# Kernel optimization log

Measured on AMD Instinct MI355X. Metric: run time of the kernel, lower is better.

The kernel has to match this reference:

```python
import jax, jax.numpy as jnp
import numpy as np

KH, KW = 7, 7      # t2t kernel_size
ST = 3             # stride
PD = 3             # padding
K = KH * KW        # 49 taps per patch


def _patch_indices(H, W):
    """Linear indices into the padded (Hp,Wp) image for every (patch l, tap k)."""
    Hp, Wp = H + 2 * PD, W + 2 * PD
    oh = (H + 2 * PD - KH) // ST + 1
    ow = (W + 2 * PD - KW) // ST + 1
    ki, kj = np.meshgrid(np.arange(KH), np.arange(KW), indexing='ij')
    rows = (np.arange(oh) * ST)[:, None, None, None] + ki[None, None]   # (oh,1,kh,kw)
    cols = (np.arange(ow) * ST)[None, :, None, None] + kj[None, None]   # (1,ow,kh,kw)
    idx = (rows * Wp + cols).reshape(oh * ow, K)                        # (L, 49)
    return jnp.asarray(idx), Hp, Wp, oh * ow


def setup_inputs() -> dict:
    key = jax.random.key(0)
    k1, k2, k3 = jax.random.split(key, 3)
    b, n, d, hd = 2, 5760, 512, 1960
    return {
        'x': jax.random.normal(k1, (b, n, d), dtype=jnp.float32),
        'W1': jax.random.normal(k2, (d, hd), dtype=jnp.float32) * 0.02,
        'b1': jnp.zeros((hd,), dtype=jnp.float32),
        'W2': jax.random.normal(k3, (hd, d), dtype=jnp.float32) * 0.02,
        'b2': jnp.zeros((d,), dtype=jnp.float32),
        'out_h': 60,
        'out_w': 108,
    }


def reference(x, W1, b1, W2, b2, out_h, out_w):
    H, W = int(out_h), int(out_w)
    idx, Hp, Wp, L = _patch_indices(H, W)          # idx: (L, 49)
    idxf = idx.reshape(-1)                         # (L*49,)

    b, n, _ = x.shape
    h = x @ W1 + b1                                # (b, n, 1960)
    hd = h.shape[-1]
    C = hd // K                                    # 40 fold channels
    Bp = (b * n) // L                              # fold batch (= b * t)

    # fold input layout: (Bp, C, K, L) -> scatter-add into padded image
    patches = h.reshape(Bp, L, C, K)
    vals = jnp.transpose(patches, (0, 2, 1, 3)).reshape(Bp * C, L * K)
    img = jnp.zeros((Bp * C, Hp * Wp), x.dtype).at[:, idxf].add(vals)

    # overlap-count normalizer (fold of ones), same for every batch/channel
    count = jnp.zeros((Hp * Wp,), x.dtype).at[idxf].add(jnp.ones_like(idxf, x.dtype))

    # crop padding (as F.fold does), normalize, re-pad with zeros (as F.unfold does)
    img = img.reshape(Bp, C, Hp, Wp)[:, :, PD:PD + H, PD:PD + W]
    cnt = count.reshape(Hp, Wp)[PD:PD + H, PD:PD + W]
    img = img / cnt
    flat = jnp.pad(img, ((0, 0), (0, 0), (PD, PD), (PD, PD))).reshape(Bp * C, Hp * Wp)

    # unfold: gather the same taps back, restore (b, n, hd) token layout
    g = flat[:, idxf].reshape(Bp, C, L, K)
    g = jnp.transpose(g, (0, 2, 1, 3)).reshape(b, n, hd)

    return jax.nn.gelu(g, approximate=False) @ W2 + b2
```

## Files before the change

### kernel.cpp

```cpp
#include <hip/hip_runtime.h>

typedef _Float16 f16;
typedef __attribute__((ext_vector_type(8))) _Float16 half8;
typedef __attribute__((ext_vector_type(4))) _Float16 half4;
typedef __attribute__((ext_vector_type(4))) float f32x4;

#define LDS_AS __attribute__((address_space(3)))
#define GLB_AS __attribute__((address_space(1)))

__device__ __forceinline__ void load16_lds(const f16* g, f16* l) {
    __builtin_amdgcn_global_load_lds((GLB_AS void*)(g), (LDS_AS void*)(l), 16, 0, 0);
}

#define WAIT4_BARRIER()  asm volatile("s_waitcnt vmcnt(4)\n\ts_barrier" ::: "memory")
#define WAIT0_BARRIER()  asm volatile("s_waitcnt vmcnt(0)\n\ts_barrier" ::: "memory")
#define PLAIN_BARRIER()  asm volatile("s_barrier" ::: "memory")

__global__ __launch_bounds__(256, 2) void gemm1(
    const f16* __restrict__ A, const f16* __restrict__ Bt,
    const float* __restrict__ bias, f16* __restrict__ C)
{
    const int id  = blockIdx.x;
    const int xcd = id & 7;
    const int r   = id >> 3;
    const int mt  = r & 15;
    const int nt  = xcd + 8 * (r >> 4);
    if (nt >= 90) return;
    const int m0 = mt * 128, n0 = nt * 128;
    const int K = 512, ldc = 11520;

    __shared__ f16 As[2][128 * 32];
    __shared__ f16 Bs[2][128 * 32];
    const int tid  = threadIdx.x;
    const int wave = tid >> 6;
    const int lane = tid & 63;

    const int s0 = tid, s1 = tid + 256;
    const f16* gA0 = A  + (m0 + (s0 >> 2)) * K + (s0 & 3) * 8;
    const f16* gA1 = A  + (m0 + (s1 >> 2)) * K + (s1 & 3) * 8;
    const f16* gB0 = Bt + (n0 + (s0 >> 2)) * K + (s0 & 3) * 8;
    const f16* gB1 = Bt + (n0 + (s1 >> 2)) * K + (s1 & 3) * 8;

    const int wm = (wave >> 1) * 64;
    const int wn = (wave & 1) * 64;
    const int lr = lane & 15;
    const int k8 = (lane >> 4) * 8;

    f32x4 acc[4][4];
#pragma unroll
    for (int i = 0; i < 4; ++i)
#pragma unroll
        for (int j = 0; j < 4; ++j) acc[i][j] = f32x4{0.f, 0.f, 0.f, 0.f};

#define G1_ISSUE(st, k0) do { \
    load16_lds(gA0 + (k0), &As[st][wave * 512]); \
    load16_lds(gA1 + (k0), &As[st][2048 + wave * 512]); \
    load16_lds(gB0 + (k0), &Bs[st][wave * 512]); \
    load16_lds(gB1 + (k0), &Bs[st][2048 + wave * 512]); \
} while (0)

    G1_ISSUE(0, 0);
    const int NS = 16;
    for (int s = 0; s < NS; ++s) {
        const int cur = s & 1;
        if (s + 1 < NS) {
            G1_ISSUE(cur ^ 1, (s + 1) * 32);
            WAIT4_BARRIER();
        } else {
            WAIT0_BARRIER();
        }
        half8 af[4], bf[4];
#pragma unroll
        for (int i = 0; i < 4; ++i)
            af[i] = *(const half8*)&As[cur][(wm + i * 16 + lr) * 32 + k8];
#pragma unroll
        for (int j = 0; j < 4; ++j)
            bf[j] = *(const half8*)&Bs[cur][(wn + j * 16 + lr) * 32 + k8];
#pragma unroll
        for (int i = 0; i < 4; ++i)
#pragma unroll
            for (int j = 0; j < 4; ++j)
                acc[i][j] = __builtin_amdgcn_mfma_f32_16x16x32_f16(
                    af[i], bf[j], acc[i][j], 0, 0, 0);
        PLAIN_BARRIER();
    }

#pragma unroll
    for (int i = 0; i < 4; ++i) {
#pragma unroll
        for (int rr = 0; rr < 4; ++rr) {
            const int row = m0 + wm + i * 16 + (lane >> 4) * 4 + rr;
            const float bvr = (row < 1960) ? bias[row] : 0.f;
#pragma unroll
            for (int j = 0; j < 4; ++j) {
                const int col = n0 + wn + j * 16 + lr;
                C[row * ldc + col] = (f16)(acc[i][j][rr] + bvr);
            }
        }
    }
}

__global__ __launch_bounds__(512, 2) void gemm2(
    const f16* __restrict__ A, const f16* __restrict__ Bt,
    const float* __restrict__ bias, float* __restrict__ Cout)
{
    const int id  = blockIdx.x;
    const int xcd = id & 7;
    const int j2  = id >> 3;
    const int nt  = j2 & 3;
    const int mt  = (j2 >> 2) * 8 + xcd;
    if (mt >= 90) return;
    const int m0 = mt * 128, n0 = nt * 128;

    __shared__ f16 smem[32768];
    const int tid  = threadIdx.x;
    const int half = tid >> 8;
    const int t    = tid & 255;
    const int wave = (tid >> 6) & 3;
    const int lane = tid & 63;

    const int kbase = half * 1024;
    const int s1 = t + 256;
    const f16* gA0 = A  + (m0 + (t  >> 2)) * 2048 + kbase + (t  & 3) * 8;
    const f16* gA1 = A  + (m0 + (s1 >> 2)) * 2048 + kbase + (s1 & 3) * 8;
    const f16* gB0 = Bt + (n0 + (t  >> 2)) * 2048 + kbase + (t  & 3) * 8;
    const f16* gB1 = Bt + (n0 + (s1 >> 2)) * 2048 + kbase + (s1 & 3) * 8;
    f16* hb = &smem[half * 16384];

    const int wm = (wave >> 1) * 64;
    const int wn = (wave & 1) * 64;
    const int lr = lane & 15;
    const int k8 = (lane >> 4) * 8;

    f32x4 acc[4][4];
#pragma unroll
    for (int i = 0; i < 4; ++i)
#pragma unroll
        for (int j = 0; j < 4; ++j) acc[i][j] = f32x4{0.f, 0.f, 0.f, 0.f};

#define G2_ISSUE(st, k0) do { \
    f16* sb = hb + (st) * 8192; \
    load16_lds(gA0 + (k0), sb + wave * 512); \
    load16_lds(gA1 + (k0), sb + 2048 + wave * 512); \
    load16_lds(gB0 + (k0), sb + 4096 + wave * 512); \
    load16_lds(gB1 + (k0), sb + 6144 + wave * 512); \
} while (0)

    G2_ISSUE(0, 0);
    const int NS = 32;
    for (int s = 0; s < NS; ++s) {
        const int cur = s & 1;
        if (s + 1 < NS) {
            G2_ISSUE(cur ^ 1, (s + 1) * 32);
            WAIT4_BARRIER();
        } else {
            WAIT0_BARRIER();
        }
        const f16* sa = hb + cur * 8192;
        const f16* sbB = sa + 4096;
        half8 af[4], bf[4];
#pragma unroll
        for (int i = 0; i < 4; ++i)
            af[i] = *(const half8*)&sa[(wm + i * 16 + lr) * 32 + k8];
#pragma unroll
        for (int j = 0; j < 4; ++j)
            bf[j] = *(const half8*)&sbB[(wn + j * 16 + lr) * 32 + k8];
#pragma unroll
        for (int i = 0; i < 4; ++i)
#pragma unroll
            for (int j = 0; j < 4; ++j)
                acc[i][j] = __builtin_amdgcn_mfma_f32_16x16x32_f16(
                    af[i], bf[j], acc[i][j], 0, 0, 0);
        PLAIN_BARRIER();
    }

    float* accl = (float*)smem;
    if (half == 1) {
#pragma unroll
        for (int i = 0; i < 4; ++i)
#pragma unroll
            for (int rr = 0; rr < 4; ++rr) {
                const int row = wm + i * 16 + (lane >> 4) * 4 + rr;
#pragma unroll
                for (int j = 0; j < 4; ++j)
                    accl[row * 128 + wn + j * 16 + lr] = acc[i][j][rr];
            }
    }
    __syncthreads();
    if (half == 0) {
#pragma unroll
        for (int j = 0; j < 4; ++j) {
            const int col = wn + j * 16 + lr;
            const float bv = bias[n0 + col];
#pragma unroll
            for (int i = 0; i < 4; ++i) {
#pragma unroll
                for (int rr = 0; rr < 4; ++rr) {
                    const int row = wm + i * 16 + (lane >> 4) * 4 + rr;
                    Cout[(m0 + row) * 512 + n0 + col] =
                        acc[i][j][rr] + accl[row * 128 + col] + bv;
                }
            }
        }
    }
}

__global__ void fold_gelu(const f16* __restrict__ h_t, f16* __restrict__ imgG)
{
    const int r  = blockIdx.x;
    const int bc = blockIdx.y;
    const int bp  = bc / 40;
    const int cch = bc % 40;
    const int c = threadIdx.x;
    if (c >= 114) return;
    float outv = 0.f;
    if (r >= 3 && r < 63 && c >= 3 && c < 111) {
        const int qr = r / 3, rm = r % 3;
        const int qc = c / 3, cm = c % 3;
        int kis[3], ohs[3], nr = 0;
        int kjs[3], ows[3], nc = 0;
#pragma unroll
        for (int t = 0; t < 3; ++t) {
            const int ki = rm + 3 * t, oh = qr - t;
            if (ki < 7 && oh >= 0 && oh < 20) { kis[nr] = ki; ohs[nr] = oh; ++nr; }
            const int kj = cm + 3 * t, ow = qc - t;
            if (kj < 7 && ow >= 0 && ow < 36) { kjs[nc] = kj; ows[nc] = ow; ++nc; }
        }
        float sum = 0.f;
        for (int a = 0; a < nr; ++a)
            for (int b = 0; b < nc; ++b) {
                const int n = cch * 49 + kis[a] * 7 + kjs[b];
                const int token = bp * 720 + ohs[a] * 36 + ows[b];
                sum += (float)h_t[n * 11520 + token];
            }
        const float xv = sum / (float)(nr * nc);
        outv = 0.5f * xv * (1.f + erff(xv * 0.70710678118654752f));
    }
    imgG[(bc * 66 + r) * 114 + c] = (f16)outv;
}

__global__ __launch_bounds__(256) void unfold_lds(
    const f16* __restrict__ imgG, f16* __restrict__ g16)
{
    __shared__ f16 ch[7524];
    const int bc = blockIdx.x;
    const int bp = bc / 40, cch = bc % 40;
    const float* src = (const float*)(imgG + bc * 7524);
    float* dst = (float*)ch;
    for (int i = threadIdx.x; i < 3762; i += 256) dst[i] = src[i];
    __syncthreads();
    const int tokbase = bp * 720;
    const int colbase = cch * 49;
    for (int flat = threadIdx.x; flat < 35280; flat += 256) {
        const int l = flat / 49, k = flat - l * 49;
        const int oh = l / 36, ow = l - oh * 36;
        const int ki = k / 7,  kj = k - ki * 7;
        g16[(tokbase + l) * 2048 + colbase + k] =
            ch[(oh * 3 + ki) * 114 + ow * 3 + kj];
    }
    if (cch >= 36) {
        const int cb = 1960 + (cch - 36) * 22;
        for (int flat = threadIdx.x; flat < 720 * 22; flat += 256) {
            const int l = flat / 22, k = flat - l * 22;
            g16[(tokbase + l) * 2048 + cb + k] = (f16)0.f;
        }
    }
}

__global__ void cvt_x(const float* __restrict__ x, f16* __restrict__ xh, int n4)
{
    const int i = blockIdx.x * 256 + threadIdx.x;
    if (i < n4) {
        const float4 v = ((const float4*)x)[i];
        half4 o;
        o[0] = (f16)v.x; o[1] = (f16)v.y; o[2] = (f16)v.z; o[3] = (f16)v.w;
        ((half4*)xh)[i] = o;
    }
}

__global__ void transpose_pad(const float* __restrict__ src, f16* __restrict__ dst,
                              int R, int C, int Rp, int Cp)
{
    __shared__ float tile[32][33];
    const int r0 = blockIdx.x * 32, c0 = blockIdx.y * 32;
    const int tx = threadIdx.x, ty = threadIdx.y;
#pragma unroll
    for (int i = 0; i < 32; i += 8) {
        const int r = r0 + ty + i, c = c0 + tx;
        tile[ty + i][tx] = (r < R && c < C) ? src[r * C + c] : 0.f;
    }
    __syncthreads();
#pragma unroll
    for (int i = 0; i < 32; i += 8) {
        const int c = c0 + ty + i, r = r0 + tx;
        if (c < Cp && r < Rp) dst[c * Rp + r] = (f16)tile[tx][ty + i];
    }
}

extern "C" void kernel_launch(void* const* d_in, const int* in_sizes, int n_in,
                              void* d_out, int out_size, void* d_ws, size_t ws_size,
                              hipStream_t stream)
{
    const float* x  = (const float*)d_in[0];
    const float* W1 = (const float*)d_in[1];
    const float* b1 = (const float*)d_in[2];
    const float* W2 = (const float*)d_in[3];
    const float* b2 = (const float*)d_in[4];

    char* ws = (char*)d_ws;
    f16* xh   = (f16*)(ws);
    f16* W1t  = (f16*)(ws + 11796480);
    f16* W2t  = (f16*)(ws + 11796480 + 2097152);
    f16* hbuf = (f16*)(ws + 11796480 + 2 * 2097152);
    f16* imgG = (f16*)(ws + 11796480 + 2 * 2097152 + 47185920);

    cvt_x<<<dim3(5760), dim3(256), 0, stream>>>(x, xh, 1474560);
    transpose_pad<<<dim3(16, 64), dim3(32, 8), 0, stream>>>(W1, W1t, 512, 1960, 512, 2048);
    transpose_pad<<<dim3(64, 16), dim3(32, 8), 0, stream>>>(W2, W2t, 1960, 512, 2048, 512);
    gemm1<<<dim3(1536), dim3(256), 0, stream>>>(W1t, xh, b1, hbuf);
    fold_gelu<<<dim3(66, 640), dim3(128), 0, stream>>>(hbuf, imgG);
    unfold_lds<<<dim3(640), dim3(256), 0, stream>>>(imgG, hbuf);
    gemm2<<<dim3(384), dim3(512), 0, stream>>>(hbuf, W2t, b2, (float*)d_out);
}
```

Before: 234.7 us.

## Halve gemm2 N tile, raise occupancy bounds, merge prep kernels into one launch

gemm2 now uses 128x64 output tiles with 768 blocks instead of 128x128 with 384, cutting LDS and accumulator registers per block and raising the launch-bounds occupancy hint. The goal is to fill more CUs and hide latency on a GEMM that otherwise launches few blocks. gemm1's occupancy hint goes from 2 to 3. The x conversion and two weight transposes are merged into one launch to remove launch overhead. The cost is more redundant A-tile loads in gemm2, a simpler block mapping that drops the XCD-aware swizzle, and possible register spills under the tighter bounds.

```diff
diff --git a/kernel.cpp b/kernel.cpp
--- a/kernel.cpp
+++ b/kernel.cpp
@@ -13,10 +13,11 @@
 }
 
 #define WAIT4_BARRIER()  asm volatile("s_waitcnt vmcnt(4)\n\ts_barrier" ::: "memory")
+#define WAIT3_BARRIER()  asm volatile("s_waitcnt vmcnt(3)\n\ts_barrier" ::: "memory")
 #define WAIT0_BARRIER()  asm volatile("s_waitcnt vmcnt(0)\n\ts_barrier" ::: "memory")
 #define PLAIN_BARRIER()  asm volatile("s_barrier" ::: "memory")
 
-__global__ __launch_bounds__(256, 2) void gemm1(
+__global__ __launch_bounds__(256, 3) void gemm1(
     const f16* __restrict__ A, const f16* __restrict__ Bt,
     const float* __restrict__ bias, f16* __restrict__ C)
 {
@@ -100,19 +101,17 @@
     }
 }
 
-__global__ __launch_bounds__(512, 2) void gemm2(
+__global__ __launch_bounds__(512, 4) void gemm2(
     const f16* __restrict__ A, const f16* __restrict__ Bt,
     const float* __restrict__ bias, float* __restrict__ Cout)
 {
-    const int id  = blockIdx.x;
-    const int xcd = id & 7;
-    const int j2  = id >> 3;
-    const int nt  = j2 & 3;
-    const int mt  = (j2 >> 2) * 8 + xcd;
+    const int id = blockIdx.x;
+    const int nt = id / 96;
+    const int mt = id % 96;
     if (mt >= 90) return;
-    const int m0 = mt * 128, n0 = nt * 128;
-
-    __shared__ f16 smem[32768];
+    const int m0 = mt * 128, n0 = nt * 64;
+
+    __shared__ f16 smem[24576];
     const int tid  = threadIdx.x;
     const int half = tid >> 8;
     const int t    = tid & 255;
@@ -124,26 +123,24 @@
     const f16* gA0 = A  + (m0 + (t  >> 2)) * 2048 + kbase + (t  & 3) * 8;
     const f16* gA1 = A  + (m0 + (s1 >> 2)) * 2048 + kbase + (s1 & 3) * 8;
     const f16* gB0 = Bt + (n0 + (t  >> 2)) * 2048 + kbase + (t  & 3) * 8;
-    const f16* gB1 = Bt + (n0 + (s1 >> 2)) * 2048 + kbase + (s1 & 3) * 8;
-    f16* hb = &smem[half * 16384];
+    f16* hb = &smem[half * 12288];
 
     const int wm = (wave >> 1) * 64;
-    const int wn = (wave & 1) * 64;
+    const int wn = (wave & 1) * 32;
     const int lr = lane & 15;
     const int k8 = (lane >> 4) * 8;
 
-    f32x4 acc[4][4];
+    f32x4 acc[4][2];
 #pragma unroll
     for (int i = 0; i < 4; ++i)
 #pragma unroll
-        for (int j = 0; j < 4; ++j) acc[i][j] = f32x4{0.f, 0.f, 0.f, 0.f};
+        for (int j = 0; j < 2; ++j) acc[i][j] = f32x4{0.f, 0.f, 0.f, 0.f};
 
 #define G2_ISSUE(st, k0) do { \
-    f16* sb = hb + (st) * 8192; \
+    f16* sb = hb + (st) * 6144; \
     load16_lds(gA0 + (k0), sb + wave * 512); \
     load16_lds(gA1 + (k0), sb + 2048 + wave * 512); \
     load16_lds(gB0 + (k0), sb + 4096 + wave * 512); \
-    load16_lds(gB1 + (k0), sb + 6144 + wave * 512); \
 } while (0)
 
     G2_ISSUE(0, 0);
@@ -152,23 +149,22 @@
         const int cur = s & 1;
         if (s + 1 < NS) {
             G2_ISSUE(cur ^ 1, (s + 1) * 32);
-            WAIT4_BARRIER();
+            WAIT3_BARRIER();
         } else {
             WAIT0_BARRIER();
         }
-        const f16* sa = hb + cur * 8192;
-        const f16* sbB = sa + 4096;
-        half8 af[4], bf[4];
+        const f16* sa = hb + cur * 6144;
+        half8 af[4], bf[2];
 #pragma unroll
         for (int i = 0; i < 4; ++i)
             af[i] = *(const half8*)&sa[(wm + i * 16 + lr) * 32 + k8];
 #pragma unroll
-        for (int j = 0; j < 4; ++j)
-            bf[j] = *(const half8*)&sbB[(wn + j * 16 + lr) * 32 + k8];
-#pragma unroll
-        for (int i = 0; i < 4; ++i)
-#pragma unroll
-            for (int j = 0; j < 4; ++j)
+        for (int j = 0; j < 2; ++j)
+            bf[j] = *(const half8*)&sa[4096 + (wn + j * 16 + lr) * 32 + k8];
+#pragma unroll
+        for (int i = 0; i < 4; ++i)
+#pragma unroll
+            for (int j = 0; j < 2; ++j)
                 acc[i][j] = __builtin_amdgcn_mfma_f32_16x16x32_f16(
                     af[i], bf[j], acc[i][j], 0, 0, 0);
         PLAIN_BARRIER();
@@ -182,14 +178,14 @@
             for (int rr = 0; rr < 4; ++rr) {
                 const int row = wm + i * 16 + (lane >> 4) * 4 + rr;
 #pragma unroll
-                for (int j = 0; j < 4; ++j)
-                    accl[row * 128 + wn + j * 16 + lr] = acc[i][j][rr];
+                for (int j = 0; j < 2; ++j)
+                    accl[row * 64 + wn + j * 16 + lr] = acc[i][j][rr];
             }
     }
     __syncthreads();
     if (half == 0) {
 #pragma unroll
-        for (int j = 0; j < 4; ++j) {
+        for (int j = 0; j < 2; ++j) {
             const int col = wn + j * 16 + lr;
             const float bv = bias[n0 + col];
 #pragma unroll
@@ -198,7 +194,7 @@
                 for (int rr = 0; rr < 4; ++rr) {
                     const int row = wm + i * 16 + (lane >> 4) * 4 + rr;
                     Cout[(m0 + row) * 512 + n0 + col] =
-                        acc[i][j][rr] + accl[row * 128 + col] + bv;
+                        acc[i][j][rr] + accl[row * 64 + col] + bv;
                 }
             }
         }
@@ -267,23 +263,33 @@
     }
 }
 
-__global__ void cvt_x(const float* __restrict__ x, f16* __restrict__ xh, int n4)
-{
-    const int i = blockIdx.x * 256 + threadIdx.x;
-    if (i < n4) {
+__global__ __launch_bounds__(256) void prep(
+    const float* __restrict__ x, f16* __restrict__ xh,
+    const float* __restrict__ W1, f16* __restrict__ W1t,
+    const float* __restrict__ W2, f16* __restrict__ W2t)
+{
+    __shared__ float tile[32][33];
+    const int b = blockIdx.x, t = threadIdx.x;
+    if (b < 5760) {
+        const int i = b * 256 + t;
         const float4 v = ((const float4*)x)[i];
         half4 o;
         o[0] = (f16)v.x; o[1] = (f16)v.y; o[2] = (f16)v.z; o[3] = (f16)v.w;
         ((half4*)xh)[i] = o;
-    }
-}
-
-__global__ void transpose_pad(const float* __restrict__ src, f16* __restrict__ dst,
-                              int R, int C, int Rp, int Cp)
-{
-    __shared__ float tile[32][33];
-    const int r0 = blockIdx.x * 32, c0 = blockIdx.y * 32;
-    const int tx = threadIdx.x, ty = threadIdx.y;
+        return;
+    }
+    const float* src; f16* dst; int R, C, Rp, Cp, bx, by;
+    if (b < 6784) {
+        const int local = b - 5760;
+        bx = local & 15; by = local >> 4;
+        src = W1; dst = W1t; R = 512; C = 1960; Rp = 512; Cp = 2048;
+    } else {
+        const int local = b - 6784;
+        bx = local & 63; by = local >> 6;
+        src = W2; dst = W2t; R = 1960; C = 512; Rp = 2048; Cp = 512;
+    }
+    const int r0 = bx * 32, c0 = by * 32;
+    const int tx = t & 31, ty = t >> 5;
 #pragma unroll
     for (int i = 0; i < 32; i += 8) {
         const int r = r0 + ty + i, c = c0 + tx;
@@ -314,11 +320,9 @@
     f16* hbuf = (f16*)(ws + 11796480 + 2 * 2097152);
     f16* imgG = (f16*)(ws + 11796480 + 2 * 2097152 + 47185920);
 
-    cvt_x<<<dim3(5760), dim3(256), 0, stream>>>(x, xh, 1474560);
-    transpose_pad<<<dim3(16, 64), dim3(32, 8), 0, stream>>>(W1, W1t, 512, 1960, 512, 2048);
-    transpose_pad<<<dim3(64, 16), dim3(32, 8), 0, stream>>>(W2, W2t, 1960, 512, 2048, 512);
+    prep<<<dim3(7808), dim3(256), 0, stream>>>(x, xh, W1, W1t, W2, W2t);
     gemm1<<<dim3(1536), dim3(256), 0, stream>>>(W1t, xh, b1, hbuf);
     fold_gelu<<<dim3(66, 640), dim3(128), 0, stream>>>(hbuf, imgG);
     unfold_lds<<<dim3(640), dim3(256), 0, stream>>>(imgG, hbuf);
-    gemm2<<<dim3(384), dim3(512), 0, stream>>>(hbuf, W2t, b2, (float*)d_out);
-}
+    gemm2<<<dim3(768), dim3(512), 0, stream>>>(hbuf, W2t, b2, (float*)d_out);
+}
```

Result: no change. 233.0 us (-0.7%).
